# Kernel optimization log

Measured on AMD Instinct MI355X. Metric: run time of the kernel, lower is better.

## Reference

```python
import jax, jax.numpy as jnp
import numpy as np

# norse default LIFParameters / LIParameters constants
DT = 1e-3
TAU_SYN_INV = 200.0
TAU_MEM_INV = 100.0
V_LEAK = 0.0
V_TH = 1.0
V_RESET = 0.0
ALPHA = 100.0  # superspike surrogate-gradient slope


@jax.custom_vjp
def superspike(x):
    return (x > 0).astype(x.dtype)

def _ss_fwd(x):
    return (x > 0).astype(x.dtype), x

def _ss_bwd(x, g):
    return (g / (ALPHA * jnp.abs(x) + 1.0) ** 2,)

superspike.defvjp(_ss_fwd, _ss_bwd)


def lif_step(state, inp):
    """norse lif_feed_forward_step: decay v/i, spike on old current, then inject input."""
    v, i = state
    v_dec = v + DT * TAU_MEM_INV * ((V_LEAK - v) + i)
    i_dec = i - DT * TAU_SYN_INV * i
    z = superspike(v_dec - V_TH)
    v_new = (1.0 - z) * v_dec + z * V_RESET
    return z, (v_new, i_dec + inp)


def li_step(state, inp):
    """norse li_feed_forward_step: leaky integrator, output is the membrane voltage."""
    v, i = state
    v_new = v + DT * TAU_MEM_INV * ((V_LEAK - v) + i)
    i_new = i - DT * TAU_SYN_INV * i + inp
    return v_new, (v_new, i_new)


def setup_inputs() -> dict:
    key = jax.random.key(0)
    ks = jax.random.split(key, 5)
    B = 65536
    x = jax.random.normal(ks[0], (B, 1, 10, 10), dtype=jnp.float32)
    conv_w = jax.random.normal(ks[1], (2, 1, 4, 4), dtype=jnp.float32) * 0.3
    conv_b = jax.random.normal(ks[2], (2,), dtype=jnp.float32) * 0.1
    fc_w = jax.random.normal(ks[3], (10, 72), dtype=jnp.float32) * 0.1
    fc_b = jax.random.normal(ks[4], (10,), dtype=jnp.float32) * 0.1
    return {"x": x, "conv_w": conv_w, "conv_b": conv_b, "fc_w": fc_w, "fc_b": fc_b, "num_steps": 64}


def reference(x, conv_w, conv_b, fc_w, fc_b, num_steps):
    B = x.shape[0]
    out_dim = fc_w.shape[0]
    # static input: conv(x) identical at every step, hoist out of the time loop
    g = jax.lax.conv_general_dilated(
        x, conv_w, (1, 1), "VALID",
        dimension_numbers=("NCHW", "OIHW", "NCHW"),
    ) + conv_b[None, :, None, None]  # [B,2,7,7]

    def pool(z):  # MaxPool2d(kernel=2, stride=1), VALID
        return jax.lax.reduce_window(
            z, -jnp.inf, jax.lax.max, (1, 1, 2, 2), (1, 1, 1, 1), "VALID")

    s_lif0 = (jnp.zeros_like(g), jnp.zeros_like(g))                 # [B,2,7,7]
    s_li1_0 = (jnp.zeros((B, 2, 6, 6), x.dtype), jnp.zeros((B, 2, 6, 6), x.dtype))
    s_li2_0 = (jnp.zeros((B, out_dim), x.dtype), jnp.zeros((B, out_dim), x.dtype))

    def step(carry, _):
        s_lif, s1, s2 = carry
        z, s_lif = lif_step(s_lif, g)          # spikes [B,2,7,7]
        z = pool(z)                            # [B,2,6,6]
        z, s1 = li_step(s1, z)                 # LI voltage [B,2,6,6]
        z = z.reshape(B, -1)                   # [B,72]
        z = z @ fc_w.T + fc_b                  # [B,10]
        v, s2 = li_step(s2, z)                 # readout voltage [B,10]
        return (s_lif, s1, s2), None

    (s_lif, s1, s2), _ = jax.lax.scan(step, (s_lif0, s_li1_0, s_li2_0), None, length=num_steps)
    return s2[0]  # final readout membrane voltage [B, output_size]
```

## Files before the change

### kernel.cpp

```cpp
#include <hip/hip_runtime.h>

#define TMAX 64

__global__ __launch_bounds__(256) void snn_fused(
    const float* __restrict__ x,
    const float* __restrict__ conv_w,
    const float* __restrict__ conv_b,
    const float* __restrict__ fc_w,
    const float* __restrict__ fc_b,
    const int*   __restrict__ nsteps,
    float*       __restrict__ out,
    int B)
{
    __shared__ double d_F[TMAX];
    __shared__ float  s_r[TMAX];
    __shared__ float  s_rb[TMAX];
    __shared__ float  s_tab[8][256];
    __shared__ float  s_fcw[720];
    __shared__ float  s_fcb[16];
    __shared__ float  s_cb;

    const int tid = threadIdx.x;
    int T = nsteps[0];
    if (T > TMAX) T = TMAX;
    if (T < 0) T = 0;
    const int tlo = T < 32 ? T : 32;
    const int thi = T > 32 ? (T - 32) : 0;

    if (tid < TMAX) {
        double p9 = 1.0, p8 = 1.0;
        for (int k = 0; k < tid; ++k) { p9 *= 0.9; p8 *= 0.8; }
        d_F[tid] = p9 - p8;
    }
    for (int idx = tid; idx < 720; idx += 256) s_fcw[idx] = fc_w[idx];
    if (tid < 10) s_fcb[tid] = fc_b[tid];
    __syncthreads();

    if (tid < TMAX) {
        double r = 0.0;
        if (tid < T) {
            const int n = T - 1 - tid;
            for (int u = 0; u <= n; ++u) r += d_F[n - u] * d_F[u];
        }
        s_r[tid] = (float)r;
    }
    if (tid == 0) {
        double cb = 0.0;
        for (int m = 0; m < T; ++m) cb += d_F[m];
        s_cb = (float)cb;
    }
    __syncthreads();

    if (tid < 32) {
        s_rb[tid] = (tid < tlo) ? s_r[tlo - 1 - tid] : 0.f;
    } else if (tid < 64) {
        const int p = tid - 32;
        s_rb[tid] = (p < thi) ? s_r[tlo + thi - 1 - p] : 0.f;
    }
    __syncthreads();

    {
        const int v8 = tid;
        #pragma unroll
        for (int k = 0; k < 8; ++k) {
            float ssum = 0.f;
            #pragma unroll
            for (int bb = 0; bb < 8; ++bb)
                if ((v8 >> bb) & 1) ssum += s_rb[k * 8 + bb];
            s_tab[k][v8] = ssum;
        }
    }
    __syncthreads();

    const float cbsum = s_cb;

    const int gt = blockIdx.x * 256 + tid;
    const int h = gt & 1;
    const int c = (gt >> 1) & 1;
    const int b = gt >> 2;
    if (b >= B) return;

    const float* xb = x + b * 100;

    float wc[16];
    {
        const float4* wq = reinterpret_cast<const float4*>(conv_w + c * 16);
        #pragma unroll
        for (int k = 0; k < 4; ++k) {
            float4 t = wq[k];
            wc[4*k+0] = t.x; wc[4*k+1] = t.y; wc[4*k+2] = t.z; wc[4*k+3] = t.w;
        }
    }
    const float cbias = conv_b[c];

    float outacc[10];
    #pragma unroll
    for (int o = 0; o < 10; ++o) outacc[o] = 0.f;

    unsigned int plo[7], phi[7];
    float fzero = 0.0f;

    const int ybase = 3 * h;

    for (int r = 0; r < 4; ++r) {
        const int y = ybase + r;

        float gg7[7];
        #pragma unroll
        for (int xx = 0; xx < 7; ++xx) gg7[xx] = 0.f;
        #pragma unroll
        for (int ky = 0; ky < 4; ++ky) {
            float xrow[10];
            const float2* q = reinterpret_cast<const float2*>(xb + (y + ky) * 10);
            #pragma unroll
            for (int k = 0; k < 5; ++k) { float2 t = q[k]; xrow[2*k] = t.x; xrow[2*k+1] = t.y; }
            #pragma unroll
            for (int xx = 0; xx < 7; ++xx) {
                float a = gg7[xx];
                #pragma unroll
                for (int kx = 0; kx < 4; ++kx)
                    a = __fadd_rn(a, __fmul_rn(wc[ky*4 + kx], xrow[xx + kx]));
                gg7[xx] = a;
            }
        }
        #pragma unroll
        for (int xx = 0; xx < 7; ++xx) gg7[xx] = __fadd_rn(gg7[xx], cbias);

        float v[7], ii[7];
        unsigned int mlo[7], mhi[7];
        #pragma unroll
        for (int xx = 0; xx < 7; ++xx) { v[xx] = 0.f; ii[xx] = 0.f; mlo[xx] = 0u; mhi[xx] = 0u; }

        #pragma unroll 4
        for (int t = 0; t < tlo; ++t) {
            #pragma unroll
            for (int xx = 0; xx < 7; ++xx) {
                const float imv  = __fsub_rn(ii[xx], v[xx]);
                const float vdec = __fadd_rn(v[xx], __fmul_rn(0.1f, imv));
                const float idec = __fsub_rn(ii[xx], __fmul_rn(0.2f, ii[xx]));
                float vnew;
                asm("v_cmp_lt_f32 vcc, 1.0, %[vd]\n\t"
                    "v_cndmask_b32 %[vn], %[vd], %[vz], vcc\n\t"
                    "v_addc_co_u32 %[mm], vcc, %[mm], %[mm], vcc"
                    : [vn]"=v"(vnew), [mm]"+v"(mlo[xx])
                    : [vd]"v"(vdec), [vz]"v"(fzero)
                    : "vcc");
                v[xx]  = vnew;
                ii[xx] = __fadd_rn(idec, gg7[xx]);
            }
        }
        #pragma unroll 4
        for (int t = 0; t < thi; ++t) {
            #pragma unroll
            for (int xx = 0; xx < 7; ++xx) {
                const float imv  = __fsub_rn(ii[xx], v[xx]);
                const float vdec = __fadd_rn(v[xx], __fmul_rn(0.1f, imv));
                const float idec = __fsub_rn(ii[xx], __fmul_rn(0.2f, ii[xx]));
                float vnew;
                asm("v_cmp_lt_f32 vcc, 1.0, %[vd]\n\t"
                    "v_cndmask_b32 %[vn], %[vd], %[vz], vcc\n\t"
                    "v_addc_co_u32 %[mm], vcc, %[mm], %[mm], vcc"
                    : [vn]"=v"(vnew), [mm]"+v"(mhi[xx])
                    : [vd]"v"(vdec), [vz]"v"(fzero)
                    : "vcc");
                v[xx]  = vnew;
                ii[xx] = __fadd_rn(idec, gg7[xx]);
            }
        }

        if (r > 0) {
            const int py = ybase + r - 1;
            const int jbase = c * 36 + py * 6;
            #pragma unroll
            for (int px = 0; px < 6; ++px) {
                const unsigned int pl = plo[px] | plo[px+1] | mlo[px] | mlo[px+1];
                const unsigned int ph = phi[px] | phi[px+1] | mhi[px] | mhi[px+1];
                float a = s_tab[0][pl & 255] + s_tab[1][(pl >> 8) & 255]
                        + s_tab[2][(pl >> 16) & 255] + s_tab[3][pl >> 24]
                        + s_tab[4][ph & 255] + s_tab[5][(ph >> 8) & 255]
                        + s_tab[6][(ph >> 16) & 255] + s_tab[7][ph >> 24];
                const int j = jbase + px;
                #pragma unroll
                for (int o = 0; o < 10; ++o)
                    outacc[o] = fmaf(s_fcw[o * 72 + j], a, outacc[o]);
            }
        }
        #pragma unroll
        for (int xx = 0; xx < 7; ++xx) { plo[xx] = mlo[xx]; phi[xx] = mhi[xx]; }
    }

    #pragma unroll
    for (int o = 0; o < 10; ++o) {
        float t1  = outacc[o] + __shfl_xor(outacc[o], 1);
        float tot = t1 + __shfl_xor(t1, 2);
        tot = fmaf(cbsum, s_fcb[o], tot);
        if ((gt & 3) == 0) out[b * 10 + o] = tot;
    }
}

extern "C" void kernel_launch(void* const* d_in, const int* in_sizes, int n_in,
                              void* d_out, int out_size, void* d_ws, size_t ws_size,
                              hipStream_t stream) {
    const float* x      = (const float*)d_in[0];
    const float* conv_w = (const float*)d_in[1];
    const float* conv_b = (const float*)d_in[2];
    const float* fc_w   = (const float*)d_in[3];
    const float* fc_b   = (const float*)d_in[4];
    const int*   nsteps = (const int*)d_in[5];
    float* outp = (float*)d_out;

    const int B = in_sizes[0] / 100;
    const int total = 4 * B;
    const int block = 256;
    const int grid = (total + block - 1) / block;
    snn_fused<<<grid, block, 0, stream>>>(x, conv_w, conv_b, fc_w, fc_b, nsteps, outp, B);
}
```

Measured before the change: 91.05 us.

## Assign one conv row per thread and pool across lanes via shuffles

Each batch element is now handled by 16 threads instead of 4. Each thread computes one conv output row for one channel and runs that row's LIF recurrence. Each thread used to walk four rows in sequence. Vertical max-pooling now reads the neighbouring row's spike masks with __shfl_down instead of carrying the previous row's masks in registers, and the readout is reduced over 16 lanes. This raises thread-level parallelism and shortens each thread's serial chain. In exchange it launches four times as many blocks, each repeating the double-precision table setup, and one of every 8 lanes computes a duplicate row that produces no output.

Result: faster. 83.30 us (-8.5%).

```diff
diff --git a/kernel.cpp b/kernel.cpp
--- a/kernel.cpp
+++ b/kernel.cpp
@@ -74,44 +74,32 @@
 
     const float cbsum = s_cb;
 
-    const int gt = blockIdx.x * 256 + tid;
-    const int h = gt & 1;
-    const int c = (gt >> 1) & 1;
-    const int b = gt >> 2;
+    const int gt  = blockIdx.x * 256 + tid;
+    const int sub = gt & 15;
+    const int b   = gt >> 4;
+    const int c   = sub >> 3;
+    const int y   = sub & 7;
+    const int ysim = (y < 6) ? y : 6;
     if (b >= B) return;
 
     const float* xb = x + b * 100;
-
-    float wc[16];
+    const float cbias = conv_b[c];
+
+    float gg7[7];
+    #pragma unroll
+    for (int xx = 0; xx < 7; ++xx) gg7[xx] = 0.f;
     {
+        float wc[16];
         const float4* wq = reinterpret_cast<const float4*>(conv_w + c * 16);
         #pragma unroll
         for (int k = 0; k < 4; ++k) {
             float4 t = wq[k];
             wc[4*k+0] = t.x; wc[4*k+1] = t.y; wc[4*k+2] = t.z; wc[4*k+3] = t.w;
         }
-    }
-    const float cbias = conv_b[c];
-
-    float outacc[10];
-    #pragma unroll
-    for (int o = 0; o < 10; ++o) outacc[o] = 0.f;
-
-    unsigned int plo[7], phi[7];
-    float fzero = 0.0f;
-
-    const int ybase = 3 * h;
-
-    for (int r = 0; r < 4; ++r) {
-        const int y = ybase + r;
-
-        float gg7[7];
-        #pragma unroll
-        for (int xx = 0; xx < 7; ++xx) gg7[xx] = 0.f;
         #pragma unroll
         for (int ky = 0; ky < 4; ++ky) {
             float xrow[10];
-            const float2* q = reinterpret_cast<const float2*>(xb + (y + ky) * 10);
+            const float2* q = reinterpret_cast<const float2*>(xb + (ysim + ky) * 10);
             #pragma unroll
             for (int k = 0; k < 5; ++k) { float2 t = q[k]; xrow[2*k] = t.x; xrow[2*k+1] = t.y; }
             #pragma unroll
@@ -123,78 +111,89 @@
                 gg7[xx] = a;
             }
         }
-        #pragma unroll
-        for (int xx = 0; xx < 7; ++xx) gg7[xx] = __fadd_rn(gg7[xx], cbias);
-
-        float v[7], ii[7];
-        unsigned int mlo[7], mhi[7];
-        #pragma unroll
-        for (int xx = 0; xx < 7; ++xx) { v[xx] = 0.f; ii[xx] = 0.f; mlo[xx] = 0u; mhi[xx] = 0u; }
-
-        #pragma unroll 4
-        for (int t = 0; t < tlo; ++t) {
-            #pragma unroll
-            for (int xx = 0; xx < 7; ++xx) {
-                const float imv  = __fsub_rn(ii[xx], v[xx]);
-                const float vdec = __fadd_rn(v[xx], __fmul_rn(0.1f, imv));
-                const float idec = __fsub_rn(ii[xx], __fmul_rn(0.2f, ii[xx]));
-                float vnew;
-                asm("v_cmp_lt_f32 vcc, 1.0, %[vd]\n\t"
-                    "v_cndmask_b32 %[vn], %[vd], %[vz], vcc\n\t"
-                    "v_addc_co_u32 %[mm], vcc, %[mm], %[mm], vcc"
-                    : [vn]"=v"(vnew), [mm]"+v"(mlo[xx])
-                    : [vd]"v"(vdec), [vz]"v"(fzero)
-                    : "vcc");
-                v[xx]  = vnew;
-                ii[xx] = __fadd_rn(idec, gg7[xx]);
-            }
-        }
-        #pragma unroll 4
-        for (int t = 0; t < thi; ++t) {
-            #pragma unroll
-            for (int xx = 0; xx < 7; ++xx) {
-                const float imv  = __fsub_rn(ii[xx], v[xx]);
-                const float vdec = __fadd_rn(v[xx], __fmul_rn(0.1f, imv));
-                const float idec = __fsub_rn(ii[xx], __fmul_rn(0.2f, ii[xx]));
-                float vnew;
-                asm("v_cmp_lt_f32 vcc, 1.0, %[vd]\n\t"
-                    "v_cndmask_b32 %[vn], %[vd], %[vz], vcc\n\t"
-                    "v_addc_co_u32 %[mm], vcc, %[mm], %[mm], vcc"
-                    : [vn]"=v"(vnew), [mm]"+v"(mhi[xx])
-                    : [vd]"v"(vdec), [vz]"v"(fzero)
-                    : "vcc");
-                v[xx]  = vnew;
-                ii[xx] = __fadd_rn(idec, gg7[xx]);
-            }
-        }
-
-        if (r > 0) {
-            const int py = ybase + r - 1;
-            const int jbase = c * 36 + py * 6;
-            #pragma unroll
-            for (int px = 0; px < 6; ++px) {
-                const unsigned int pl = plo[px] | plo[px+1] | mlo[px] | mlo[px+1];
-                const unsigned int ph = phi[px] | phi[px+1] | mhi[px] | mhi[px+1];
-                float a = s_tab[0][pl & 255] + s_tab[1][(pl >> 8) & 255]
-                        + s_tab[2][(pl >> 16) & 255] + s_tab[3][pl >> 24]
-                        + s_tab[4][ph & 255] + s_tab[5][(ph >> 8) & 255]
-                        + s_tab[6][(ph >> 16) & 255] + s_tab[7][ph >> 24];
-                const int j = jbase + px;
-                #pragma unroll
-                for (int o = 0; o < 10; ++o)
-                    outacc[o] = fmaf(s_fcw[o * 72 + j], a, outacc[o]);
-            }
-        }
-        #pragma unroll
-        for (int xx = 0; xx < 7; ++xx) { plo[xx] = mlo[xx]; phi[xx] = mhi[xx]; }
+    }
+    #pragma unroll
+    for (int xx = 0; xx < 7; ++xx) gg7[xx] = __fadd_rn(gg7[xx], cbias);
+
+    float v[7], ii[7];
+    unsigned int mlo[7], mhi[7];
+    float fzero = 0.0f;
+    #pragma unroll
+    for (int xx = 0; xx < 7; ++xx) { v[xx] = 0.f; ii[xx] = 0.f; mlo[xx] = 0u; mhi[xx] = 0u; }
+
+    #pragma unroll 4
+    for (int t = 0; t < tlo; ++t) {
+        #pragma unroll
+        for (int xx = 0; xx < 7; ++xx) {
+            const float imv  = __fsub_rn(ii[xx], v[xx]);
+            const float vdec = __fadd_rn(v[xx], __fmul_rn(0.1f, imv));
+            const float idec = __fsub_rn(ii[xx], __fmul_rn(0.2f, ii[xx]));
+            float vnew;
+            asm("v_cmp_lt_f32 vcc, 1.0, %[vd]\n\t"
+                "v_cndmask_b32 %[vn], %[vd], %[vz], vcc\n\t"
+                "v_addc_co_u32 %[mm], vcc, %[mm], %[mm], vcc"
+                : [vn]"=v"(vnew), [mm]"+v"(mlo[xx])
+                : [vd]"v"(vdec), [vz]"v"(fzero)
+                : "vcc");
+            v[xx]  = vnew;
+            ii[xx] = __fadd_rn(idec, gg7[xx]);
+        }
+    }
+    #pragma unroll 4
+    for (int t = 0; t < thi; ++t) {
+        #pragma unroll
+        for (int xx = 0; xx < 7; ++xx) {
+            const float imv  = __fsub_rn(ii[xx], v[xx]);
+            const float vdec = __fadd_rn(v[xx], __fmul_rn(0.1f, imv));
+            const float idec = __fsub_rn(ii[xx], __fmul_rn(0.2f, ii[xx]));
+            float vnew;
+            asm("v_cmp_lt_f32 vcc, 1.0, %[vd]\n\t"
+                "v_cndmask_b32 %[vn], %[vd], %[vz], vcc\n\t"
+                "v_addc_co_u32 %[mm], vcc, %[mm], %[mm], vcc"
+                : [vn]"=v"(vnew), [mm]"+v"(mhi[xx])
+                : [vd]"v"(vdec), [vz]"v"(fzero)
+                : "vcc");
+            v[xx]  = vnew;
+            ii[xx] = __fadd_rn(idec, gg7[xx]);
+        }
+    }
+
+    unsigned int nlo[7], nhi[7];
+    #pragma unroll
+    for (int xx = 0; xx < 7; ++xx) {
+        nlo[xx] = __shfl_down(mlo[xx], 1);
+        nhi[xx] = __shfl_down(mhi[xx], 1);
+    }
+
+    float outacc[10];
+    #pragma unroll
+    for (int o = 0; o < 10; ++o) outacc[o] = 0.f;
+
+    if (y < 6) {
+        const int jbase = c * 36 + y * 6;
+        #pragma unroll
+        for (int px = 0; px < 6; ++px) {
+            const unsigned int pl = mlo[px] | mlo[px+1] | nlo[px] | nlo[px+1];
+            const unsigned int ph = mhi[px] | mhi[px+1] | nhi[px] | nhi[px+1];
+            float a = s_tab[0][pl & 255] + s_tab[1][(pl >> 8) & 255]
+                    + s_tab[2][(pl >> 16) & 255] + s_tab[3][pl >> 24]
+                    + s_tab[4][ph & 255] + s_tab[5][(ph >> 8) & 255]
+                    + s_tab[6][(ph >> 16) & 255] + s_tab[7][ph >> 24];
+            const int j = jbase + px;
+            #pragma unroll
+            for (int o = 0; o < 10; ++o)
+                outacc[o] = fmaf(s_fcw[o * 72 + j], a, outacc[o]);
+        }
     }
 
     #pragma unroll
     for (int o = 0; o < 10; ++o) {
-        float t1  = outacc[o] + __shfl_xor(outacc[o], 1);
-        float tot = t1 + __shfl_xor(t1, 2);
-        tot = fmaf(cbsum, s_fcb[o], tot);
-        if ((gt & 3) == 0) out[b * 10 + o] = tot;
+        float t = outacc[o];
+        t += __shfl_xor(t, 1);
+        t += __shfl_xor(t, 2);
+        t += __shfl_xor(t, 4);
+        t += __shfl_xor(t, 8);
+        if (sub == 0) out[b * 10 + o] = fmaf(cbsum, s_fcb[o], t);
     }
 }
 
@@ -210,7 +209,7 @@
     float* outp = (float*)d_out;
 
     const int B = in_sizes[0] / 100;
-    const int total = 4 * B;
+    const int total = 16 * B;
     const int block = 256;
     const int grid = (total + block - 1) / block;
     snn_fused<<<grid, block, 0, stream>>>(x, conv_w, conv_b, fc_w, fc_b, nsteps, outp, B);
```
